# Kernel tuning notes

Measured on AMD Instinct MI355X. Metric: run time of the kernel, lower is better.

## Reference

```python
import jax, jax.numpy as jnp
import numpy as np

NUM_ITERATIONS = 3
LAMBDA_WEIGHT = 0.6
EPS = 1e-8


def _squash(s):
    # s: [N, out_dim]; norm over feature dim (dim=1 in torch, keepdim)
    s_norm = jnp.linalg.norm(s, axis=1, keepdims=True)
    scale = s_norm / (1.0 + s_norm)
    return scale * s / (s_norm + EPS)


def setup_inputs() -> dict:
    key = jax.random.key(0)
    k_h, k_adj, k_w, k_a = jax.random.split(key, 4)
    N, in_dim, out_dim = 4096, 128, 128
    h = jax.random.normal(k_h, (N, in_dim), dtype=jnp.float32)
    adj = jax.random.uniform(k_adj, (N, N), dtype=jnp.float32)
    # xavier_uniform for W [in_dim, out_dim] and attn_a [2*out_dim, 1]
    lim_w = float(np.sqrt(6.0 / (in_dim + out_dim)))
    W = jax.random.uniform(k_w, (in_dim, out_dim), minval=-lim_w, maxval=lim_w, dtype=jnp.float32)
    lim_a = float(np.sqrt(6.0 / (2 * out_dim + 1)))
    attn_a = jax.random.uniform(k_a, (2 * out_dim, 1), minval=-lim_a, maxval=lim_a, dtype=jnp.float32)
    return {"h": h, "adj": adj, "W": W, "attn_a": attn_a}


def reference(h, adj, W, attn_a):
    # Symmetric degree normalization
    d = adj.sum(axis=1) + 1e-8
    d_inv_sqrt = 1.0 / jnp.sqrt(d)
    adj_norm = d_inv_sqrt[:, None] * adj * d_inv_sqrt[None, :]  # [N, N]

    u_hat = h @ W  # [N, out_dim]

    # GAT-style scores via additive decomposition (same math as cat+matmul,
    # avoids the O(N^2 * 2d) h_concat tensor):
    out_dim = W.shape[1]
    a_src = attn_a[:out_dim, 0]  # [in_dim] (in_dim == out_dim)
    a_dst = attn_a[out_dim:, 0]
    attn_scores = (h @ a_src)[:, None] + (h @ a_dst)[None, :]  # [N, N]
    attn_weights = jax.nn.leaky_relu(attn_scores, negative_slope=0.2)

    # Dynamic routing
    b = adj_norm
    c = None
    for it in range(NUM_ITERATIONS):
        c = jax.nn.softmax(b, axis=1)  # [N, N]
        s = c @ u_hat                  # [N, out_dim]
        v = _squash(s)
        if it < NUM_ITERATIONS - 1:
            b = b + v @ u_hat.T        # agreement [N, N]

    combined = LAMBDA_WEIGHT * c + (1.0 - LAMBDA_WEIGHT) * jax.nn.softmax(attn_weights, axis=1)
    s = combined @ u_hat
    return _squash(s)
```

## Files before the change

### kernel.cpp

```cpp
#include <hip/hip_runtime.h>
#include <hip/hip_bf16.h>
#include <math.h>

#define N 4096
#define D 128
#define EPSV 1e-8f

typedef __attribute__((ext_vector_type(8))) short bf16x8;
typedef __attribute__((ext_vector_type(4))) float f32x4;

__device__ __forceinline__ float lrelu(float x){ return x > 0.f ? x : 0.2f*x; }

__device__ __forceinline__ ushort bf16_hi(float x){
  __hip_bfloat16 h = __float2bfloat16(x);
  return *reinterpret_cast<ushort*>(&h);
}
__device__ __forceinline__ float bf16_tof(ushort u){
  __hip_bfloat16 h = *reinterpret_cast<__hip_bfloat16*>(&u);
  return __bfloat162float(h);
}

__device__ __forceinline__ float wave_sum(float v){
  #pragma unroll
  for (int off = 32; off; off >>= 1) v += __shfl_down(v, off);
  return v;
}
__device__ __forceinline__ float block_sum256(float v, float* red){
  v = wave_sum(v);
  if ((threadIdx.x & 63) == 0) red[threadIdx.x >> 6] = v;
  __syncthreads();
  float r = (red[0] + red[1]) + (red[2] + red[3]);
  __syncthreads();
  return r;
}

__global__ void k_rowsum(const float* __restrict__ adj, float* __restrict__ dis){
  int i = blockIdx.x;
  const float4* row = reinterpret_cast<const float4*>(adj + (size_t)i * N);
  float s = 0.f;
  #pragma unroll
  for (int l = 0; l < 4; ++l){
    float4 v = row[threadIdx.x + l * 256];
    s += (v.x + v.y) + (v.z + v.w);
  }
  __shared__ float red[4];
  s = block_sum256(s, red);
  if (threadIdx.x == 0) dis[i] = 1.0f / sqrtf(s + EPSV);
}

__global__ void k_uhat2(const float* __restrict__ h, const float* __restrict__ W,
                        const float* __restrict__ aa,
                        ushort* __restrict__ u_hi, ushort* __restrict__ u_lo,
                        float* __restrict__ p, float* __restrict__ q){
  int i = blockIdx.x, t = threadIdx.x;
  __shared__ float hs[D];
  __shared__ float red[4];
  float hv = h[(size_t)i * D + t];
  hs[t] = hv;
  __syncthreads();
  float acc = 0.f;
  #pragma unroll 8
  for (int k = 0; k < D; ++k) acc = fmaf(hs[k], W[k * D + t], acc);
  ushort hh = bf16_hi(acc);
  u_hi[(size_t)i * D + t] = hh;
  u_lo[(size_t)i * D + t] = bf16_hi(acc - bf16_tof(hh));
  float pv = hv * aa[t];
  float qv = hv * aa[D + t];
  pv = wave_sum(pv); qv = wave_sum(qv);
  if ((t & 63) == 0){ red[t >> 6] = pv; red[2 + (t >> 6)] = qv; }
  __syncthreads();
  if (t == 0){ p[i] = red[0] + red[1]; q[i] = red[2] + red[3]; }
}

__global__ void k_transposeU2(const ushort* __restrict__ u_hi, const ushort* __restrict__ u_lo,
                              ushort* __restrict__ uT_pk){
  __shared__ ushort T[64][136];
  const int tid = threadIdx.x;
  const int j0 = blockIdx.x * 64;
  for (int pass = 0; pass < 2; ++pass){
    const ushort* s = pass ? u_lo : u_hi;
    __syncthreads();
    #pragma unroll
    for (int l = 0; l < 4; ++l){
      int r = l * 16 + (tid >> 4);
      int c = (tid & 15) * 8;
      *reinterpret_cast<uint4*>(&T[r][c]) =
          *reinterpret_cast<const uint4*>(s + (size_t)(j0 + r) * D + c);
    }
    __syncthreads();
    const int dd = tid >> 1, half = tid & 1;
    #pragma unroll
    for (int g = 0; g < 4; ++g){
      int jb = half * 32 + g * 8;
      uint w0 = (uint)T[jb+0][dd] | ((uint)T[jb+1][dd] << 16);
      uint w1 = (uint)T[jb+2][dd] | ((uint)T[jb+3][dd] << 16);
      uint w2 = (uint)T[jb+4][dd] | ((uint)T[jb+5][dd] << 16);
      uint w3 = (uint)T[jb+6][dd] | ((uint)T[jb+7][dd] << 16);
      uint4 w; w.x = w0; w.y = w1; w.z = w2; w.w = w3;
      size_t off = ((size_t)dd * (N/8) + ((j0 + jb) >> 3)) * 16 + pass * 8;
      *reinterpret_cast<uint4*>(uT_pk + off) = w;
    }
  }
}

template<int MODE>
__global__ __launch_bounds__(256, 4)
void k_gemm4(const float* __restrict__ src, const float* __restrict__ dis,
             const float* __restrict__ p, const float* __restrict__ q,
             const ushort* __restrict__ uT_pk,
             float* __restrict__ s_part, float* __restrict__ l_part, int kRange)
{
  const int lane = threadIdx.x & 63;
  const int wave = threadIdx.x >> 6;
  const int row0 = blockIdx.x * 64 + wave * 16;
  const int cl   = lane & 15;
  const int kgrp = (lane >> 4) * 8;
  const int arow = row0 + cl;
  const int k0b  = blockIdx.y * kRange;

  const float dif = (MODE == 0) ? dis[arow] : 0.f;
  const float pi  = (MODE == 2) ? p[arow] : 0.f;
  const float* srow = (MODE == 2) ? q : src + (size_t)arow * N;

  f32x4 acc[8] = {};
  float lsum = 0.f;

  float av[8], dv[8];
  {
    int kk = k0b + kgrp;
    *reinterpret_cast<float4*>(av)     = *reinterpret_cast<const float4*>(srow + kk);
    *reinterpret_cast<float4*>(av + 4) = *reinterpret_cast<const float4*>(srow + kk + 4);
    if (MODE == 0){
      *reinterpret_cast<float4*>(dv)     = *reinterpret_cast<const float4*>(dis + kk);
      *reinterpret_cast<float4*>(dv + 4) = *reinterpret_cast<const float4*>(dis + kk + 4);
    }
  }

  for (int kt = 0; kt < kRange; kt += 32){
    const int kk = k0b + kt + kgrp;
    float4 n0, n1, m0, m1;
    const bool more = (kt + 32 < kRange);
    if (more){
      n0 = *reinterpret_cast<const float4*>(srow + kk + 32);
      n1 = *reinterpret_cast<const float4*>(srow + kk + 36);
      if (MODE == 0){
        m0 = *reinterpret_cast<const float4*>(dis + kk + 32);
        m1 = *reinterpret_cast<const float4*>(dis + kk + 36);
      }
    }
    float ex[8];
    #pragma unroll
    for (int e = 0; e < 8; ++e){
      float x;
      if (MODE == 0)      x = av[e] * dif * dv[e];
      else if (MODE == 1) x = av[e];
      else                x = lrelu(pi + av[e]);
      ex[e] = __expf(x);
      lsum += ex[e];
    }
    bf16x8 ahi, alo;
    #pragma unroll
    for (int e = 0; e < 8; ++e){
      ushort hh = bf16_hi(ex[e]);
      ahi[e] = (short)hh;
      alo[e] = (short)bf16_hi(ex[e] - bf16_tof(hh));
    }
    const size_t kb16 = (size_t)(kk >> 3) * 16;
    #pragma unroll
    for (int ct = 0; ct < 8; ++ct){
      const ushort* bp = uT_pk + (size_t)(ct * 16 + cl) * (N/8) * 16 + kb16;
      bf16x8 bh = *reinterpret_cast<const bf16x8*>(bp);
      bf16x8 bl = *reinterpret_cast<const bf16x8*>(bp + 8);
      acc[ct] = __builtin_amdgcn_mfma_f32_16x16x32_bf16(ahi, bh, acc[ct], 0, 0, 0);
      acc[ct] = __builtin_amdgcn_mfma_f32_16x16x32_bf16(ahi, bl, acc[ct], 0, 0, 0);
      acc[ct] = __builtin_amdgcn_mfma_f32_16x16x32_bf16(alo, bh, acc[ct], 0, 0, 0);
    }
    if (more){
      *reinterpret_cast<float4*>(av)     = n0;
      *reinterpret_cast<float4*>(av + 4) = n1;
      if (MODE == 0){
        *reinterpret_cast<float4*>(dv)     = m0;
        *reinterpret_cast<float4*>(dv + 4) = m1;
      }
    }
  }

  lsum += __shfl_xor(lsum, 16);
  lsum += __shfl_xor(lsum, 32);
  if (lane < 16) l_part[(size_t)blockIdx.y * N + row0 + lane] = lsum;

  const int orow = row0 + (lane >> 4) * 4;
  float* sp = s_part + ((size_t)blockIdx.y * N + orow) * D + cl;
  #pragma unroll
  for (int ct = 0; ct < 8; ++ct)
    #pragma unroll
    for (int r = 0; r < 4; ++r)
      sp[(size_t)r * D + ct * 16] = acc[ct][r];
}

__global__ void k_reduce_attn(const float* __restrict__ s_part, const float* __restrict__ l_part,
                              float* __restrict__ s_attn, float* __restrict__ l_a, int ks){
  int row = blockIdx.x, t = threadIdx.x;
  float a = 0.f;
  for (int y = 0; y < ks; ++y) a += s_part[((size_t)y * N + row) * D + t];
  s_attn[(size_t)row * D + t] = a;
  if (t == 0){
    float la = 0.f;
    for (int y = 0; y < ks; ++y) la += l_part[(size_t)y * N + row];
    l_a[row] = la;
  }
}

template<bool FINAL>
__global__ void k_reduce_squash3(const float* __restrict__ s_part, const float* __restrict__ l_part,
                                 const float* __restrict__ s_attn, const float* __restrict__ l_a,
                                 float* __restrict__ out,
                                 ushort* __restrict__ vh, ushort* __restrict__ vl, int ks){
  int row = blockIdx.x, t = threadIdx.x;
  float a = 0.f;
  for (int y = 0; y < ks; ++y) a += s_part[((size_t)y * N + row) * D + t];
  __shared__ float lbs;
  __shared__ float red[2];
  if (t == 0){
    float lb = 0.f;
    for (int y = 0; y < ks; ++y) lb += l_part[(size_t)y * N + row];
    lbs = lb;
  }
  __syncthreads();
  float val;
  if (FINAL)
    val = 0.6f * a / lbs + 0.4f * s_attn[(size_t)row * D + t] / l_a[row];
  else
    val = a / lbs;
  float ss = wave_sum(val * val);
  if ((t & 63) == 0) red[t >> 6] = ss;
  __syncthreads();
  float tot = red[0] + red[1];
  float n = sqrtf(tot);
  float f = n / ((1.0f + n) * (n + EPSV));
  float o = val * f;
  if (FINAL) out[(size_t)row * D + t] = o;
  else {
    ushort hh = bf16_hi(o);
    vh[(size_t)row * D + t] = hh;
    vl[(size_t)row * D + t] = bf16_hi(o - bf16_tof(hh));
  }
}

template<bool FIRST>
__global__ __launch_bounds__(256, 4)
void k_bupd3(const ushort* __restrict__ v_hi, const ushort* __restrict__ v_lo,
             const ushort* __restrict__ u_hi, const ushort* __restrict__ u_lo,
             const float* __restrict__ adj, const float* __restrict__ dis,
             float* __restrict__ b)
{
  const int lane = threadIdx.x & 63;
  const int wave = threadIdx.x >> 6;
  const int row0 = (blockIdx.x >> 5) * 128 + wave * 32;
  const int col0 = (blockIdx.x & 31) * 128;
  const int cl   = lane & 15;
  const int kgrp = (lane >> 4) * 8;

  f32x4 acc[2][8] = {};

  #pragma unroll
  for (int ks = 0; ks < 4; ++ks){
    const int kk = ks * 32 + kgrp;
    bf16x8 a_h[2], a_l[2];
    #pragma unroll
    for (int rt = 0; rt < 2; ++rt){
      size_t off = (size_t)(row0 + rt * 16 + cl) * D + kk;
      a_h[rt] = *reinterpret_cast<const bf16x8*>(v_hi + off);
      a_l[rt] = *reinterpret_cast<const bf16x8*>(v_lo + off);
    }
    #pragma unroll
    for (int ct = 0; ct < 8; ++ct){
      size_t off = (size_t)(col0 + ct * 16 + cl) * D + kk;
      bf16x8 b_h = *reinterpret_cast<const bf16x8*>(u_hi + off);
      bf16x8 b_l = *reinterpret_cast<const bf16x8*>(u_lo + off);
      #pragma unroll
      for (int rt = 0; rt < 2; ++rt){
        acc[rt][ct] = __builtin_amdgcn_mfma_f32_16x16x32_bf16(a_h[rt], b_h, acc[rt][ct], 0, 0, 0);
        acc[rt][ct] = __builtin_amdgcn_mfma_f32_16x16x32_bf16(a_h[rt], b_l, acc[rt][ct], 0, 0, 0);
        acc[rt][ct] = __builtin_amdgcn_mfma_f32_16x16x32_bf16(a_l[rt], b_h, acc[rt][ct], 0, 0, 0);
      }
    }
  }

  float dcol[8];
  if (FIRST){
    #pragma unroll
    for (int ct = 0; ct < 8; ++ct) dcol[ct] = dis[col0 + ct * 16 + cl];
  }
  #pragma unroll
  for (int rt = 0; rt < 2; ++rt){
    const int orow = row0 + rt * 16 + (lane >> 4) * 4;
    #pragma unroll
    for (int r = 0; r < 4; ++r){
      const int gr = orow + r;
      const float drow = FIRST ? dis[gr] : 0.f;
      size_t base = (size_t)gr * N + col0 + cl;
      #pragma unroll
      for (int ct = 0; ct < 8; ++ct){
        size_t idx = base + ct * 16;
        if (FIRST) b[idx] = fmaf(adj[idx], drow * dcol[ct], acc[rt][ct][r]);
        else       b[idx] += acc[rt][ct][r];
      }
    }
  }
}

extern "C" void kernel_launch(void* const* d_in, const int* in_sizes, int n_in,
                              void* d_out, int out_size, void* d_ws, size_t ws_size,
                              hipStream_t stream) {
  const float* h   = (const float*)d_in[0];
  const float* adj = (const float*)d_in[1];
  const float* W   = (const float*)d_in[2];
  const float* aa  = (const float*)d_in[3];
  float* out = (float*)d_out;
  float* ws  = (float*)d_ws;

  float* dis    = ws;
  float* p      = ws + 4096;
  float* q      = ws + 8192;
  float* l_a    = ws + 12288;
  float* l_part = ws + 16384;
  ushort* u_hi  = (ushort*)(ws + 81920);
  ushort* u_lo  = u_hi  + (size_t)N * D;
  ushort* uT_pk = u_lo  + (size_t)N * D;
  ushort* v_hi  = uT_pk + (size_t)(N/8) * D * 16;
  ushort* v_lo  = v_hi  + (size_t)N * D;
  float* s_attn = (float*)(v_lo + (size_t)N * D);
  float* b      = s_attn + (size_t)N * D;
  float* s_part = b + (size_t)N * N;

  size_t base_floats = (size_t)(s_part - ws);
  int KS = 16;
  while (KS > 1 && (base_floats + (size_t)KS * N * D) * 4 > ws_size) KS >>= 1;
  int kRange = N / KS;
  dim3 gg(64, KS);

  k_rowsum<<<N, 256, 0, stream>>>(adj, dis);
  k_uhat2<<<N, 128, 0, stream>>>(h, W, aa, u_hi, u_lo, p, q);
  k_transposeU2<<<64, 256, 0, stream>>>(u_hi, u_lo, uT_pk);

  k_gemm4<2><<<gg, 256, 0, stream>>>(nullptr, dis, p, q, uT_pk, s_part, l_part, kRange);
  k_reduce_attn<<<N, 128, 0, stream>>>(s_part, l_part, s_attn, l_a, KS);

  k_gemm4<0><<<gg, 256, 0, stream>>>(adj, dis, p, q, uT_pk, s_part, l_part, kRange);
  k_reduce_squash3<false><<<N, 128, 0, stream>>>(s_part, l_part, s_attn, l_a, out, v_hi, v_lo, KS);
  k_bupd3<true><<<1024, 256, 0, stream>>>(v_hi, v_lo, u_hi, u_lo, adj, dis, b);

  k_gemm4<1><<<gg, 256, 0, stream>>>(b, dis, p, q, uT_pk, s_part, l_part, kRange);
  k_reduce_squash3<false><<<N, 128, 0, stream>>>(s_part, l_part, s_attn, l_a, out, v_hi, v_lo, KS);
  k_bupd3<false><<<1024, 256, 0, stream>>>(v_hi, v_lo, u_hi, u_lo, adj, dis, b);

  k_gemm4<1><<<gg, 256, 0, stream>>>(b, dis, p, q, uT_pk, s_part, l_part, kRange);
  k_reduce_squash3<true><<<N, 128, 0, stream>>>(s_part, l_part, s_attn, l_a, out, v_hi, v_lo, KS);
}
```

Baseline: 552.2 us.

## Stage GEMM operands through LDS and coalesce b-update stores via shared transpose

The softmax-GEMM kernel now processes 128 rows per block, cooperatively loading the A tile and the packed U^T tile into shared memory with coalesced loads. Each wave computes two row tiles, so every B fragment is reused twice, and the grid shrinks by half. The b-update kernel stages the V and U hi/lo tiles in LDS and writes results through a padded shared transpose, so global reads and writes of adj and b become coalesced float4 accesses. The cost is extra __syncthreads barriers, more LDS usage, and the loss of the previous register prefetch and explicit occupancy hint.

```diff
diff --git a/kernel.cpp b/kernel.cpp
--- a/kernel.cpp
+++ b/kernel.cpp
@@ -104,98 +104,141 @@
 }
 
 template<int MODE>
-__global__ __launch_bounds__(256, 4)
-void k_gemm4(const float* __restrict__ src, const float* __restrict__ dis,
+__global__ __launch_bounds__(256)
+void k_gemm5(const float* __restrict__ src, const float* __restrict__ dis,
              const float* __restrict__ p, const float* __restrict__ q,
              const ushort* __restrict__ uT_pk,
              float* __restrict__ s_part, float* __restrict__ l_part, int kRange)
 {
-  const int lane = threadIdx.x & 63;
-  const int wave = threadIdx.x >> 6;
-  const int row0 = blockIdx.x * 64 + wave * 16;
+  __shared__ float  As[128][36];
+  __shared__ ushort Bs[128][72];
+
+  const int tid  = threadIdx.x;
+  const int lane = tid & 63;
+  const int wave = tid >> 6;
+  const int row0 = blockIdx.x * 128;
   const int cl   = lane & 15;
   const int kgrp = (lane >> 4) * 8;
-  const int arow = row0 + cl;
   const int k0b  = blockIdx.y * kRange;
 
-  const float dif = (MODE == 0) ? dis[arow] : 0.f;
-  const float pi  = (MODE == 2) ? p[arow] : 0.f;
-  const float* srow = (MODE == 2) ? q : src + (size_t)arow * N;
-
-  f32x4 acc[8] = {};
-  float lsum = 0.f;
-
-  float av[8], dv[8];
-  {
-    int kk = k0b + kgrp;
-    *reinterpret_cast<float4*>(av)     = *reinterpret_cast<const float4*>(srow + kk);
-    *reinterpret_cast<float4*>(av + 4) = *reinterpret_cast<const float4*>(srow + kk + 4);
+  float dif[2], pr[2];
+  #pragma unroll
+  for (int rt = 0; rt < 2; ++rt){
+    int ar = row0 + wave * 32 + rt * 16 + cl;
+    dif[rt] = (MODE == 0) ? dis[ar] : 0.f;
+    pr[rt]  = (MODE == 2) ? p[ar] : 0.f;
+  }
+
+  f32x4 acc[2][8] = {};
+  float lsum[2] = {0.f, 0.f};
+
+  for (int kt = 0; kt < kRange; kt += 32){
+    const int kb = k0b + kt;
+    float4 a_st[4];
+    if (MODE != 2){
+      #pragma unroll
+      for (int i = 0; i < 4; ++i){
+        int idx = i * 256 + tid;
+        int r = idx >> 3, c = idx & 7;
+        a_st[i] = *reinterpret_cast<const float4*>(src + (size_t)(row0 + r) * N + kb + c * 4);
+      }
+    }
+    uint4 b_st[4];
+    const int kb8 = kb >> 3;
+    #pragma unroll
+    for (int i = 0; i < 4; ++i){
+      int idx = i * 256 + tid;
+      int n = idx >> 3, u = idx & 7;
+      b_st[i] = *reinterpret_cast<const uint4*>(
+          uT_pk + (size_t)n * (N/8) * 16 + (size_t)(kb8 + (u & 3)) * 16 + (u >> 2) * 8);
+    }
+    __syncthreads();
+    if (MODE != 2){
+      #pragma unroll
+      for (int i = 0; i < 4; ++i){
+        int idx = i * 256 + tid;
+        int r = idx >> 3, c = idx & 7;
+        *reinterpret_cast<float4*>(&As[r][c * 4]) = a_st[i];
+      }
+    }
+    #pragma unroll
+    for (int i = 0; i < 4; ++i){
+      int idx = i * 256 + tid;
+      int n = idx >> 3, u = idx & 7;
+      *reinterpret_cast<uint4*>(&Bs[n][(u >> 2) * 32 + (u & 3) * 8]) = b_st[i];
+    }
+    __syncthreads();
+
+    float aux[8];
     if (MODE == 0){
-      *reinterpret_cast<float4*>(dv)     = *reinterpret_cast<const float4*>(dis + kk);
-      *reinterpret_cast<float4*>(dv + 4) = *reinterpret_cast<const float4*>(dis + kk + 4);
-    }
-  }
-
-  for (int kt = 0; kt < kRange; kt += 32){
-    const int kk = k0b + kt + kgrp;
-    float4 n0, n1, m0, m1;
-    const bool more = (kt + 32 < kRange);
-    if (more){
-      n0 = *reinterpret_cast<const float4*>(srow + kk + 32);
-      n1 = *reinterpret_cast<const float4*>(srow + kk + 36);
-      if (MODE == 0){
-        m0 = *reinterpret_cast<const float4*>(dis + kk + 32);
-        m1 = *reinterpret_cast<const float4*>(dis + kk + 36);
-      }
-    }
-    float ex[8];
-    #pragma unroll
-    for (int e = 0; e < 8; ++e){
-      float x;
-      if (MODE == 0)      x = av[e] * dif * dv[e];
-      else if (MODE == 1) x = av[e];
-      else                x = lrelu(pi + av[e]);
-      ex[e] = __expf(x);
-      lsum += ex[e];
-    }
-    bf16x8 ahi, alo;
-    #pragma unroll
-    for (int e = 0; e < 8; ++e){
-      ushort hh = bf16_hi(ex[e]);
-      ahi[e] = (short)hh;
-      alo[e] = (short)bf16_hi(ex[e] - bf16_tof(hh));
-    }
-    const size_t kb16 = (size_t)(kk >> 3) * 16;
+      *reinterpret_cast<float4*>(aux)     = *reinterpret_cast<const float4*>(dis + kb + kgrp);
+      *reinterpret_cast<float4*>(aux + 4) = *reinterpret_cast<const float4*>(dis + kb + kgrp + 4);
+    } else if (MODE == 2){
+      *reinterpret_cast<float4*>(aux)     = *reinterpret_cast<const float4*>(q + kb + kgrp);
+      *reinterpret_cast<float4*>(aux + 4) = *reinterpret_cast<const float4*>(q + kb + kgrp + 4);
+    }
+
+    bf16x8 ahi[2], alo[2];
+    #pragma unroll
+    for (int rt = 0; rt < 2; ++rt){
+      float ex[8];
+      if (MODE == 2){
+        #pragma unroll
+        for (int e = 0; e < 8; ++e) ex[e] = __expf(lrelu(pr[rt] + aux[e]));
+      } else {
+        const int rl = wave * 32 + rt * 16 + cl;
+        float av[8];
+        *reinterpret_cast<float4*>(av)     = *reinterpret_cast<const float4*>(&As[rl][kgrp]);
+        *reinterpret_cast<float4*>(av + 4) = *reinterpret_cast<const float4*>(&As[rl][kgrp + 4]);
+        if (MODE == 0){
+          #pragma unroll
+          for (int e = 0; e < 8; ++e) ex[e] = __expf(av[e] * dif[rt] * aux[e]);
+        } else {
+          #pragma unroll
+          for (int e = 0; e < 8; ++e) ex[e] = __expf(av[e]);
+        }
+      }
+      #pragma unroll
+      for (int e = 0; e < 8; ++e){
+        lsum[rt] += ex[e];
+        ushort hh = bf16_hi(ex[e]);
+        ahi[rt][e] = (short)hh;
+        alo[rt][e] = (short)bf16_hi(ex[e] - bf16_tof(hh));
+      }
+    }
+
     #pragma unroll
     for (int ct = 0; ct < 8; ++ct){
-      const ushort* bp = uT_pk + (size_t)(ct * 16 + cl) * (N/8) * 16 + kb16;
-      bf16x8 bh = *reinterpret_cast<const bf16x8*>(bp);
-      bf16x8 bl = *reinterpret_cast<const bf16x8*>(bp + 8);
-      acc[ct] = __builtin_amdgcn_mfma_f32_16x16x32_bf16(ahi, bh, acc[ct], 0, 0, 0);
-      acc[ct] = __builtin_amdgcn_mfma_f32_16x16x32_bf16(ahi, bl, acc[ct], 0, 0, 0);
-      acc[ct] = __builtin_amdgcn_mfma_f32_16x16x32_bf16(alo, bh, acc[ct], 0, 0, 0);
-    }
-    if (more){
-      *reinterpret_cast<float4*>(av)     = n0;
-      *reinterpret_cast<float4*>(av + 4) = n1;
-      if (MODE == 0){
-        *reinterpret_cast<float4*>(dv)     = m0;
-        *reinterpret_cast<float4*>(dv + 4) = m1;
-      }
-    }
-  }
-
-  lsum += __shfl_xor(lsum, 16);
-  lsum += __shfl_xor(lsum, 32);
-  if (lane < 16) l_part[(size_t)blockIdx.y * N + row0 + lane] = lsum;
-
-  const int orow = row0 + (lane >> 4) * 4;
-  float* sp = s_part + ((size_t)blockIdx.y * N + orow) * D + cl;
-  #pragma unroll
-  for (int ct = 0; ct < 8; ++ct)
-    #pragma unroll
-    for (int r = 0; r < 4; ++r)
-      sp[(size_t)r * D + ct * 16] = acc[ct][r];
+      const int col = ct * 16 + cl;
+      bf16x8 bh = *reinterpret_cast<const bf16x8*>(&Bs[col][kgrp]);
+      bf16x8 bl = *reinterpret_cast<const bf16x8*>(&Bs[col][32 + kgrp]);
+      #pragma unroll
+      for (int rt = 0; rt < 2; ++rt){
+        acc[rt][ct] = __builtin_amdgcn_mfma_f32_16x16x32_bf16(ahi[rt], bh, acc[rt][ct], 0, 0, 0);
+        acc[rt][ct] = __builtin_amdgcn_mfma_f32_16x16x32_bf16(ahi[rt], bl, acc[rt][ct], 0, 0, 0);
+        acc[rt][ct] = __builtin_amdgcn_mfma_f32_16x16x32_bf16(alo[rt], bh, acc[rt][ct], 0, 0, 0);
+      }
+    }
+  }
+
+  #pragma unroll
+  for (int rt = 0; rt < 2; ++rt){
+    float l = lsum[rt];
+    l += __shfl_xor(l, 16);
+    l += __shfl_xor(l, 32);
+    if (lane < 16)
+      l_part[(size_t)blockIdx.y * N + row0 + wave * 32 + rt * 16 + lane] = l;
+  }
+  #pragma unroll
+  for (int rt = 0; rt < 2; ++rt){
+    const int orow = row0 + wave * 32 + rt * 16 + (lane >> 4) * 4;
+    float* sp = s_part + ((size_t)blockIdx.y * N + orow) * D + cl;
+    #pragma unroll
+    for (int ct = 0; ct < 8; ++ct)
+      #pragma unroll
+      for (int r = 0; r < 4; ++r)
+        sp[(size_t)r * D + ct * 16] = acc[rt][ct][r];
+  }
 }
 
 __global__ void k_reduce_attn(const float* __restrict__ s_part, const float* __restrict__ l_part,
@@ -248,15 +291,21 @@
 }
 
 template<bool FIRST>
-__global__ __launch_bounds__(256, 4)
-void k_bupd3(const ushort* __restrict__ v_hi, const ushort* __restrict__ v_lo,
+__global__ __launch_bounds__(256)
+void k_bupd5(const ushort* __restrict__ v_hi, const ushort* __restrict__ v_lo,
              const ushort* __restrict__ u_hi, const ushort* __restrict__ u_lo,
              const float* __restrict__ adj, const float* __restrict__ dis,
              float* __restrict__ b)
 {
-  const int lane = threadIdx.x & 63;
-  const int wave = threadIdx.x >> 6;
-  const int row0 = (blockIdx.x >> 5) * 128 + wave * 32;
+  __shared__ __align__(16) char smem[36864];
+  ushort (*vs)[72] = reinterpret_cast<ushort(*)[72]>(smem);
+  ushort (*us)[72] = reinterpret_cast<ushort(*)[72]>(smem + 18432);
+  float*  tr       = reinterpret_cast<float*>(smem);
+
+  const int tid  = threadIdx.x;
+  const int lane = tid & 63;
+  const int wave = tid >> 6;
+  const int row0 = (blockIdx.x >> 5) * 128;
   const int col0 = (blockIdx.x & 31) * 128;
   const int cl   = lane & 15;
   const int kgrp = (lane >> 4) * 8;
@@ -265,19 +314,39 @@
 
   #pragma unroll
   for (int ks = 0; ks < 4; ++ks){
-    const int kk = ks * 32 + kgrp;
+    const int kk = ks * 32;
+    uint4 v_st[4], u_st[4];
+    #pragma unroll
+    for (int i = 0; i < 4; ++i){
+      int idx = i * 256 + tid;
+      int r = idx >> 3, uu = idx & 7;
+      const ushort* vsrc = (uu < 4) ? v_hi : v_lo;
+      v_st[i] = *reinterpret_cast<const uint4*>(vsrc + (size_t)(row0 + r) * D + kk + (uu & 3) * 8);
+      const ushort* usrc = (uu < 4) ? u_hi : u_lo;
+      u_st[i] = *reinterpret_cast<const uint4*>(usrc + (size_t)(col0 + r) * D + kk + (uu & 3) * 8);
+    }
+    __syncthreads();
+    #pragma unroll
+    for (int i = 0; i < 4; ++i){
+      int idx = i * 256 + tid;
+      int r = idx >> 3, uu = idx & 7;
+      *reinterpret_cast<uint4*>(&vs[r][(uu >> 2) * 32 + (uu & 3) * 8]) = v_st[i];
+      *reinterpret_cast<uint4*>(&us[r][(uu >> 2) * 32 + (uu & 3) * 8]) = u_st[i];
+    }
+    __syncthreads();
+
     bf16x8 a_h[2], a_l[2];
     #pragma unroll
     for (int rt = 0; rt < 2; ++rt){
-      size_t off = (size_t)(row0 + rt * 16 + cl) * D + kk;
-      a_h[rt] = *reinterpret_cast<const bf16x8*>(v_hi + off);
-      a_l[rt] = *reinterpret_cast<const bf16x8*>(v_lo + off);
+      const int rl = wave * 32 + rt * 16 + cl;
+      a_h[rt] = *reinterpret_cast<const bf16x8*>(&vs[rl][kgrp]);
+      a_l[rt] = *reinterpret_cast<const bf16x8*>(&vs[rl][32 + kgrp]);
     }
     #pragma unroll
     for (int ct = 0; ct < 8; ++ct){
-      size_t off = (size_t)(col0 + ct * 16 + cl) * D + kk;
-      bf16x8 b_h = *reinterpret_cast<const bf16x8*>(u_hi + off);
-      bf16x8 b_l = *reinterpret_cast<const bf16x8*>(u_lo + off);
+      const int col = ct * 16 + cl;
+      bf16x8 b_h = *reinterpret_cast<const bf16x8*>(&us[col][kgrp]);
+      bf16x8 b_l = *reinterpret_cast<const bf16x8*>(&us[col][32 + kgrp]);
       #pragma unroll
       for (int rt = 0; rt < 2; ++rt){
         acc[rt][ct] = __builtin_amdgcn_mfma_f32_16x16x32_bf16(a_h[rt], b_h, acc[rt][ct], 0, 0, 0);
@@ -285,28 +354,40 @@
         acc[rt][ct] = __builtin_amdgcn_mfma_f32_16x16x32_bf16(a_l[rt], b_h, acc[rt][ct], 0, 0, 0);
       }
     }
-  }
-
-  float dcol[8];
-  if (FIRST){
-    #pragma unroll
-    for (int ct = 0; ct < 8; ++ct) dcol[ct] = dis[col0 + ct * 16 + cl];
-  }
+    __syncthreads();
+  }
+
   #pragma unroll
   for (int rt = 0; rt < 2; ++rt){
-    const int orow = row0 + rt * 16 + (lane >> 4) * 4;
-    #pragma unroll
-    for (int r = 0; r < 4; ++r){
-      const int gr = orow + r;
-      const float drow = FIRST ? dis[gr] : 0.f;
-      size_t base = (size_t)gr * N + col0 + cl;
-      #pragma unroll
-      for (int ct = 0; ct < 8; ++ct){
-        size_t idx = base + ct * 16;
-        if (FIRST) b[idx] = fmaf(adj[idx], drow * dcol[ct], acc[rt][ct][r]);
-        else       b[idx] += acc[rt][ct][r];
-      }
-    }
+    #pragma unroll
+    for (int ct = 0; ct < 8; ++ct)
+      #pragma unroll
+      for (int r = 0; r < 4; ++r)
+        tr[(wave * 16 + (lane >> 4) * 4 + r) * 132 + ct * 16 + cl] = acc[rt][ct][r];
+    __syncthreads();
+    #pragma unroll
+    for (int i = 0; i < 8; ++i){
+      int idx = i * 256 + tid;
+      int rl = idx >> 5, c4 = (idx & 31) * 4;
+      int grow = row0 + (rl >> 4) * 32 + rt * 16 + (rl & 15);
+      float4 v = *reinterpret_cast<const float4*>(&tr[rl * 132 + c4]);
+      size_t gidx = (size_t)grow * N + col0 + c4;
+      float4 o;
+      if (FIRST){
+        float4 ad = *reinterpret_cast<const float4*>(adj + gidx);
+        float dr = dis[grow];
+        float4 dc = *reinterpret_cast<const float4*>(dis + col0 + c4);
+        o.x = fmaf(ad.x, dr * dc.x, v.x);
+        o.y = fmaf(ad.y, dr * dc.y, v.y);
+        o.z = fmaf(ad.z, dr * dc.z, v.z);
+        o.w = fmaf(ad.w, dr * dc.w, v.w);
+      } else {
+        float4 bo = *reinterpret_cast<const float4*>(b + gidx);
+        o.x = bo.x + v.x; o.y = bo.y + v.y; o.z = bo.z + v.z; o.w = bo.w + v.w;
+      }
+      *reinterpret_cast<float4*>(b + gidx) = o;
+    }
+    __syncthreads();
   }
 }
 
@@ -338,23 +419,23 @@
   int KS = 16;
   while (KS > 1 && (base_floats + (size_t)KS * N * D) * 4 > ws_size) KS >>= 1;
   int kRange = N / KS;
-  dim3 gg(64, KS);
+  dim3 gg(32, KS);
 
   k_rowsum<<<N, 256, 0, stream>>>(adj, dis);
   k_uhat2<<<N, 128, 0, stream>>>(h, W, aa, u_hi, u_lo, p, q);
   k_transposeU2<<<64, 256, 0, stream>>>(u_hi, u_lo, uT_pk);
 
-  k_gemm4<2><<<gg, 256, 0, stream>>>(nullptr, dis, p, q, uT_pk, s_part, l_part, kRange);
+  k_gemm5<2><<<gg, 256, 0, stream>>>(nullptr, dis, p, q, uT_pk, s_part, l_part, kRange);
   k_reduce_attn<<<N, 128, 0, stream>>>(s_part, l_part, s_attn, l_a, KS);
 
-  k_gemm4<0><<<gg, 256, 0, stream>>>(adj, dis, p, q, uT_pk, s_part, l_part, kRange);
+  k_gemm5<0><<<gg, 256, 0, stream>>>(adj, dis, p, q, uT_pk, s_part, l_part, kRange);
   k_reduce_squash3<false><<<N, 128, 0, stream>>>(s_part, l_part, s_attn, l_a, out, v_hi, v_lo, KS);
-  k_bupd3<true><<<1024, 256, 0, stream>>>(v_hi, v_lo, u_hi, u_lo, adj, dis, b);
-
-  k_gemm4<1><<<gg, 256, 0, stream>>>(b, dis, p, q, uT_pk, s_part, l_part, kRange);
+  k_bupd5<true><<<1024, 256, 0, stream>>>(v_hi, v_lo, u_hi, u_lo, adj, dis, b);
+
+  k_gemm5<1><<<gg, 256, 0, stream>>>(b, dis, p, q, uT_pk, s_part, l_part, kRange);
   k_reduce_squash3<false><<<N, 128, 0, stream>>>(s_part, l_part, s_attn, l_a, out, v_hi, v_lo, KS);
-  k_bupd3<false><<<1024, 256, 0, stream>>>(v_hi, v_lo, u_hi, u_lo, adj, dis, b);
-
-  k_gemm4<1><<<gg, 256, 0, stream>>>(b, dis, p, q, uT_pk, s_part, l_part, kRange);
+  k_bupd5<false><<<1024, 256, 0, stream>>>(v_hi, v_lo, u_hi, u_lo, adj, dis, b);
+
+  k_gemm5<1><<<gg, 256, 0, stream>>>(b, dis, p, q, uT_pk, s_part, l_part, kRange);
   k_reduce_squash3<true><<<N, 128, 0, stream>>>(s_part, l_part, s_attn, l_a, out, v_hi, v_lo, KS);
 }
```

New measurement: 483.0 us. -12.5%, faster.

## Fuse agreement matrix into softmax GEMM via accumulated v sum, drop b buffer

Applied to the files above, without the earlier changes.

Instead of materializing the N×N logit matrix b and updating it with separate v·uᵀ GEMMs, the routing logits are recomputed on the fly as adj_norm plus (sum of previous v)·uᵀ inside the softmax-GEMM kernel. The reduce kernel keeps a running vsum, which is split into bf16 hi/lo parts. The GEMM now stages adj and packed uᵀ tiles through shared memory. This removes the 64MB b writes and reads and the bupd kernels. In exchange it adds per-tile MFMA recomputation, extra barriers, and a fresh read of adj on every iteration.

```diff
diff --git a/kernel.cpp b/kernel.cpp
--- a/kernel.cpp
+++ b/kernel.cpp
@@ -104,98 +104,160 @@
 }
 
 template<int MODE>
-__global__ __launch_bounds__(256, 4)
-void k_gemm4(const float* __restrict__ src, const float* __restrict__ dis,
+__global__ __launch_bounds__(256)
+void k_gemm6(const float* __restrict__ adj, const float* __restrict__ dis,
              const float* __restrict__ p, const float* __restrict__ q,
              const ushort* __restrict__ uT_pk,
+             const ushort* __restrict__ u_hi, const ushort* __restrict__ u_lo,
+             const ushort* __restrict__ vs_hi, const ushort* __restrict__ vs_lo,
              float* __restrict__ s_part, float* __restrict__ l_part, int kRange)
 {
-  const int lane = threadIdx.x & 63;
-  const int wave = threadIdx.x >> 6;
-  const int row0 = blockIdx.x * 64 + wave * 16;
+  __shared__ float  As[64][36];
+  __shared__ ushort Bs[128][72];
+  __shared__ float  Cs[4][16][36];
+
+  const int tid  = threadIdx.x;
+  const int lane = tid & 63;
+  const int wave = tid >> 6;
+  const int row0 = blockIdx.x * 64;
   const int cl   = lane & 15;
   const int kgrp = (lane >> 4) * 8;
-  const int arow = row0 + cl;
   const int k0b  = blockIdx.y * kRange;
-
-  const float dif = (MODE == 0) ? dis[arow] : 0.f;
-  const float pi  = (MODE == 2) ? p[arow] : 0.f;
-  const float* srow = (MODE == 2) ? q : src + (size_t)arow * N;
+  const int arow_w = row0 + wave * 16;
+
+  const float dif = (MODE < 2) ? dis[arow_w + cl] : 0.f;
+  const float pr  = (MODE == 2) ? p[arow_w + cl] : 0.f;
 
   f32x4 acc[8] = {};
   float lsum = 0.f;
 
-  float av[8], dv[8];
-  {
-    int kk = k0b + kgrp;
-    *reinterpret_cast<float4*>(av)     = *reinterpret_cast<const float4*>(srow + kk);
-    *reinterpret_cast<float4*>(av + 4) = *reinterpret_cast<const float4*>(srow + kk + 4);
-    if (MODE == 0){
-      *reinterpret_cast<float4*>(dv)     = *reinterpret_cast<const float4*>(dis + kk);
-      *reinterpret_cast<float4*>(dv + 4) = *reinterpret_cast<const float4*>(dis + kk + 4);
-    }
-  }
-
   for (int kt = 0; kt < kRange; kt += 32){
-    const int kk = k0b + kt + kgrp;
-    float4 n0, n1, m0, m1;
-    const bool more = (kt + 32 < kRange);
-    if (more){
-      n0 = *reinterpret_cast<const float4*>(srow + kk + 32);
-      n1 = *reinterpret_cast<const float4*>(srow + kk + 36);
-      if (MODE == 0){
-        m0 = *reinterpret_cast<const float4*>(dis + kk + 32);
-        m1 = *reinterpret_cast<const float4*>(dis + kk + 36);
+    const int kb = k0b + kt;
+    float4 a_st[2];
+    if (MODE != 2){
+      #pragma unroll
+      for (int i = 0; i < 2; ++i){
+        int idx = i * 256 + tid;
+        int r = idx >> 3, c = idx & 7;
+        a_st[i] = *reinterpret_cast<const float4*>(adj + (size_t)(row0 + r) * N + kb + c * 4);
       }
     }
+    uint4 b_st[4];
+    const int kb8 = kb >> 3;
+    #pragma unroll
+    for (int i = 0; i < 4; ++i){
+      int idx = i * 256 + tid;
+      int n = idx >> 3, u = idx & 7;
+      b_st[i] = *reinterpret_cast<const uint4*>(
+          uT_pk + (size_t)n * (N/8) * 16 + (size_t)(kb8 + (u & 3)) * 16 + (u >> 2) * 8);
+    }
+    __syncthreads();
+    if (MODE != 2){
+      #pragma unroll
+      for (int i = 0; i < 2; ++i){
+        int idx = i * 256 + tid;
+        int r = idx >> 3, c = idx & 7;
+        *reinterpret_cast<float4*>(&As[r][c * 4]) = a_st[i];
+      }
+    }
+    #pragma unroll
+    for (int i = 0; i < 4; ++i){
+      int idx = i * 256 + tid;
+      int n = idx >> 3, u = idx & 7;
+      *reinterpret_cast<uint4*>(&Bs[n][(u >> 2) * 32 + (u & 3) * 8]) = b_st[i];
+    }
+    __syncthreads();
+
+    if (MODE == 1){
+      f32x4 cacc[2] = {};
+      #pragma unroll
+      for (int kk2 = 0; kk2 < D; kk2 += 32){
+        const size_t voff = (size_t)(arow_w + cl) * D + kk2 + kgrp;
+        bf16x8 vh = *reinterpret_cast<const bf16x8*>(vs_hi + voff);
+        bf16x8 vl = *reinterpret_cast<const bf16x8*>(vs_lo + voff);
+        #pragma unroll
+        for (int nt = 0; nt < 2; ++nt){
+          const size_t uoff = (size_t)(kb + nt * 16 + cl) * D + kk2 + kgrp;
+          bf16x8 uh = *reinterpret_cast<const bf16x8*>(u_hi + uoff);
+          bf16x8 ul = *reinterpret_cast<const bf16x8*>(u_lo + uoff);
+          cacc[nt] = __builtin_amdgcn_mfma_f32_16x16x32_bf16(vh, uh, cacc[nt], 0, 0, 0);
+          cacc[nt] = __builtin_amdgcn_mfma_f32_16x16x32_bf16(vh, ul, cacc[nt], 0, 0, 0);
+          cacc[nt] = __builtin_amdgcn_mfma_f32_16x16x32_bf16(vl, uh, cacc[nt], 0, 0, 0);
+        }
+      }
+      #pragma unroll
+      for (int nt = 0; nt < 2; ++nt)
+        #pragma unroll
+        for (int r = 0; r < 4; ++r)
+          Cs[wave][(lane >> 4) * 4 + r][nt * 16 + cl] = cacc[nt][r];
+      __syncthreads();
+    }
+
+    float aux[8];
+    if (MODE < 2){
+      *reinterpret_cast<float4*>(aux)     = *reinterpret_cast<const float4*>(dis + kb + kgrp);
+      *reinterpret_cast<float4*>(aux + 4) = *reinterpret_cast<const float4*>(dis + kb + kgrp + 4);
+    } else {
+      *reinterpret_cast<float4*>(aux)     = *reinterpret_cast<const float4*>(q + kb + kgrp);
+      *reinterpret_cast<float4*>(aux + 4) = *reinterpret_cast<const float4*>(q + kb + kgrp + 4);
+    }
+
     float ex[8];
+    if (MODE == 2){
+      #pragma unroll
+      for (int e = 0; e < 8; ++e) ex[e] = __expf(lrelu(pr + aux[e]));
+    } else {
+      float av[8];
+      const int rl = wave * 16 + cl;
+      *reinterpret_cast<float4*>(av)     = *reinterpret_cast<const float4*>(&As[rl][kgrp]);
+      *reinterpret_cast<float4*>(av + 4) = *reinterpret_cast<const float4*>(&As[rl][kgrp + 4]);
+      if (MODE == 1){
+        float cv[8];
+        *reinterpret_cast<float4*>(cv)     = *reinterpret_cast<const float4*>(&Cs[wave][cl][kgrp]);
+        *reinterpret_cast<float4*>(cv + 4) = *reinterpret_cast<const float4*>(&Cs[wave][cl][kgrp + 4]);
+        #pragma unroll
+        for (int e = 0; e < 8; ++e) ex[e] = __expf(av[e] * dif * aux[e] + cv[e]);
+      } else {
+        #pragma unroll
+        for (int e = 0; e < 8; ++e) ex[e] = __expf(av[e] * dif * aux[e]);
+      }
+    }
+    bf16x8 ahi, alo;
     #pragma unroll
     for (int e = 0; e < 8; ++e){
-      float x;
-      if (MODE == 0)      x = av[e] * dif * dv[e];
-      else if (MODE == 1) x = av[e];
-      else                x = lrelu(pi + av[e]);
-      ex[e] = __expf(x);
       lsum += ex[e];
-    }
-    bf16x8 ahi, alo;
-    #pragma unroll
-    for (int e = 0; e < 8; ++e){
       ushort hh = bf16_hi(ex[e]);
       ahi[e] = (short)hh;
       alo[e] = (short)bf16_hi(ex[e] - bf16_tof(hh));
     }
-    const size_t kb16 = (size_t)(kk >> 3) * 16;
+
     #pragma unroll
     for (int ct = 0; ct < 8; ++ct){
-      const ushort* bp = uT_pk + (size_t)(ct * 16 + cl) * (N/8) * 16 + kb16;
-      bf16x8 bh = *reinterpret_cast<const bf16x8*>(bp);
-      bf16x8 bl = *reinterpret_cast<const bf16x8*>(bp + 8);
+      const int col = ct * 16 + cl;
+      bf16x8 bh = *reinterpret_cast<const bf16x8*>(&Bs[col][kgrp]);
+      bf16x8 bl = *reinterpret_cast<const bf16x8*>(&Bs[col][32 + kgrp]);
       acc[ct] = __builtin_amdgcn_mfma_f32_16x16x32_bf16(ahi, bh, acc[ct], 0, 0, 0);
       acc[ct] = __builtin_amdgcn_mfma_f32_16x16x32_bf16(ahi, bl, acc[ct], 0, 0, 0);
       acc[ct] = __builtin_amdgcn_mfma_f32_16x16x32_bf16(alo, bh, acc[ct], 0, 0, 0);
     }
-    if (more){
-      *reinterpret_cast<float4*>(av)     = n0;
-      *reinterpret_cast<float4*>(av + 4) = n1;
-      if (MODE == 0){
-        *reinterpret_cast<float4*>(dv)     = m0;
-        *reinterpret_cast<float4*>(dv + 4) = m1;
-      }
-    }
-  }
-
-  lsum += __shfl_xor(lsum, 16);
-  lsum += __shfl_xor(lsum, 32);
-  if (lane < 16) l_part[(size_t)blockIdx.y * N + row0 + lane] = lsum;
-
-  const int orow = row0 + (lane >> 4) * 4;
-  float* sp = s_part + ((size_t)blockIdx.y * N + orow) * D + cl;
-  #pragma unroll
-  for (int ct = 0; ct < 8; ++ct)
-    #pragma unroll
-    for (int r = 0; r < 4; ++r)
-      sp[(size_t)r * D + ct * 16] = acc[ct][r];
+  }
+
+  {
+    float l = lsum;
+    l += __shfl_xor(l, 16);
+    l += __shfl_xor(l, 32);
+    if (lane < 16)
+      l_part[(size_t)blockIdx.y * N + arow_w + lane] = l;
+  }
+  {
+    const int orow = arow_w + (lane >> 4) * 4;
+    float* sp = s_part + ((size_t)blockIdx.y * N + orow) * D + cl;
+    #pragma unroll
+    for (int ct = 0; ct < 8; ++ct)
+      #pragma unroll
+      for (int r = 0; r < 4; ++r)
+        sp[(size_t)r * D + ct * 16] = acc[ct][r];
+  }
 }
 
 __global__ void k_reduce_attn(const float* __restrict__ s_part, const float* __restrict__ l_part,
@@ -211,11 +273,12 @@
   }
 }
 
-template<bool FINAL>
-__global__ void k_reduce_squash3(const float* __restrict__ s_part, const float* __restrict__ l_part,
-                                 const float* __restrict__ s_attn, const float* __restrict__ l_a,
-                                 float* __restrict__ out,
-                                 ushort* __restrict__ vh, ushort* __restrict__ vl, int ks){
+template<int STEP>
+__global__ void k_reduce4(const float* __restrict__ s_part, const float* __restrict__ l_part,
+                          const float* __restrict__ s_attn, const float* __restrict__ l_a,
+                          float* __restrict__ vsum,
+                          ushort* __restrict__ vh, ushort* __restrict__ vl,
+                          float* __restrict__ out, int ks){
   int row = blockIdx.x, t = threadIdx.x;
   float a = 0.f;
   for (int y = 0; y < ks; ++y) a += s_part[((size_t)y * N + row) * D + t];
@@ -227,11 +290,9 @@
     lbs = lb;
   }
   __syncthreads();
-  float val;
-  if (FINAL)
-    val = 0.6f * a / lbs + 0.4f * s_attn[(size_t)row * D + t] / l_a[row];
-  else
-    val = a / lbs;
+  float val = a / lbs;
+  if (STEP == 2)
+    val = 0.6f * val + 0.4f * s_attn[(size_t)row * D + t] / l_a[row];
   float ss = wave_sum(val * val);
   if ((t & 63) == 0) red[t >> 6] = ss;
   __syncthreads();
@@ -239,74 +300,14 @@
   float n = sqrtf(tot);
   float f = n / ((1.0f + n) * (n + EPSV));
   float o = val * f;
-  if (FINAL) out[(size_t)row * D + t] = o;
-  else {
-    ushort hh = bf16_hi(o);
+  if (STEP == 2){
+    out[(size_t)row * D + t] = o;
+  } else {
+    float nv = (STEP == 0) ? o : vsum[(size_t)row * D + t] + o;
+    vsum[(size_t)row * D + t] = nv;
+    ushort hh = bf16_hi(nv);
     vh[(size_t)row * D + t] = hh;
-    vl[(size_t)row * D + t] = bf16_hi(o - bf16_tof(hh));
-  }
-}
-
-template<bool FIRST>
-__global__ __launch_bounds__(256, 4)
-void k_bupd3(const ushort* __restrict__ v_hi, const ushort* __restrict__ v_lo,
-             const ushort* __restrict__ u_hi, const ushort* __restrict__ u_lo,
-             const float* __restrict__ adj, const float* __restrict__ dis,
-             float* __restrict__ b)
-{
-  const int lane = threadIdx.x & 63;
-  const int wave = threadIdx.x >> 6;
-  const int row0 = (blockIdx.x >> 5) * 128 + wave * 32;
-  const int col0 = (blockIdx.x & 31) * 128;
-  const int cl   = lane & 15;
-  const int kgrp = (lane >> 4) * 8;
-
-  f32x4 acc[2][8] = {};
-
-  #pragma unroll
-  for (int ks = 0; ks < 4; ++ks){
-    const int kk = ks * 32 + kgrp;
-    bf16x8 a_h[2], a_l[2];
-    #pragma unroll
-    for (int rt = 0; rt < 2; ++rt){
-      size_t off = (size_t)(row0 + rt * 16 + cl) * D + kk;
-      a_h[rt] = *reinterpret_cast<const bf16x8*>(v_hi + off);
-      a_l[rt] = *reinterpret_cast<const bf16x8*>(v_lo + off);
-    }
-    #pragma unroll
-    for (int ct = 0; ct < 8; ++ct){
-      size_t off = (size_t)(col0 + ct * 16 + cl) * D + kk;
-      bf16x8 b_h = *reinterpret_cast<const bf16x8*>(u_hi + off);
-      bf16x8 b_l = *reinterpret_cast<const bf16x8*>(u_lo + off);
-      #pragma unroll
-      for (int rt = 0; rt < 2; ++rt){
-        acc[rt][ct] = __builtin_amdgcn_mfma_f32_16x16x32_bf16(a_h[rt], b_h, acc[rt][ct], 0, 0, 0);
-        acc[rt][ct] = __builtin_amdgcn_mfma_f32_16x16x32_bf16(a_h[rt], b_l, acc[rt][ct], 0, 0, 0);
-        acc[rt][ct] = __builtin_amdgcn_mfma_f32_16x16x32_bf16(a_l[rt], b_h, acc[rt][ct], 0, 0, 0);
-      }
-    }
-  }
-
-  float dcol[8];
-  if (FIRST){
-    #pragma unroll
-    for (int ct = 0; ct < 8; ++ct) dcol[ct] = dis[col0 + ct * 16 + cl];
-  }
-  #pragma unroll
-  for (int rt = 0; rt < 2; ++rt){
-    const int orow = row0 + rt * 16 + (lane >> 4) * 4;
-    #pragma unroll
-    for (int r = 0; r < 4; ++r){
-      const int gr = orow + r;
-      const float drow = FIRST ? dis[gr] : 0.f;
-      size_t base = (size_t)gr * N + col0 + cl;
-      #pragma unroll
-      for (int ct = 0; ct < 8; ++ct){
-        size_t idx = base + ct * 16;
-        if (FIRST) b[idx] = fmaf(adj[idx], drow * dcol[ct], acc[rt][ct][r]);
-        else       b[idx] += acc[rt][ct][r];
-      }
-    }
+    vl[(size_t)row * D + t] = bf16_hi(nv - bf16_tof(hh));
   }
 }
 
@@ -324,15 +325,15 @@
   float* p      = ws + 4096;
   float* q      = ws + 8192;
   float* l_a    = ws + 12288;
-  float* l_part = ws + 16384;
-  ushort* u_hi  = (ushort*)(ws + 81920);
+  float* vsum   = ws + 16384;
+  float* l_part = vsum + (size_t)N * D;
+  ushort* u_hi  = (ushort*)(l_part + 65536);
   ushort* u_lo  = u_hi  + (size_t)N * D;
   ushort* uT_pk = u_lo  + (size_t)N * D;
-  ushort* v_hi  = uT_pk + (size_t)(N/8) * D * 16;
-  ushort* v_lo  = v_hi  + (size_t)N * D;
-  float* s_attn = (float*)(v_lo + (size_t)N * D);
-  float* b      = s_attn + (size_t)N * D;
-  float* s_part = b + (size_t)N * N;
+  ushort* vs_hi = uT_pk + (size_t)(N/8) * D * 16;
+  ushort* vs_lo = vs_hi + (size_t)N * D;
+  float* s_attn = (float*)(vs_lo + (size_t)N * D);
+  float* s_part = s_attn + (size_t)N * D;
 
   size_t base_floats = (size_t)(s_part - ws);
   int KS = 16;
@@ -344,17 +345,19 @@
   k_uhat2<<<N, 128, 0, stream>>>(h, W, aa, u_hi, u_lo, p, q);
   k_transposeU2<<<64, 256, 0, stream>>>(u_hi, u_lo, uT_pk);
 
-  k_gemm4<2><<<gg, 256, 0, stream>>>(nullptr, dis, p, q, uT_pk, s_part, l_part, kRange);
+  k_gemm6<2><<<gg, 256, 0, stream>>>(adj, dis, p, q, uT_pk, u_hi, u_lo, vs_hi, vs_lo,
+                                     s_part, l_part, kRange);
   k_reduce_attn<<<N, 128, 0, stream>>>(s_part, l_part, s_attn, l_a, KS);
 
-  k_gemm4<0><<<gg, 256, 0, stream>>>(adj, dis, p, q, uT_pk, s_part, l_part, kRange);
-  k_reduce_squash3<false><<<N, 128, 0, stream>>>(s_part, l_part, s_attn, l_a, out, v_hi, v_lo, KS);
-  k_bupd3<true><<<1024, 256, 0, stream>>>(v_hi, v_lo, u_hi, u_lo, adj, dis, b);
-
-  k_gemm4<1><<<gg, 256, 0, stream>>>(b, dis, p, q, uT_pk, s_part, l_part, kRange);
-  k_reduce_squash3<false><<<N, 128, 0, stream>>>(s_part, l_part, s_attn, l_a, out, v_hi, v_lo, KS);
-  k_bupd3<false><<<1024, 256, 0, stream>>>(v_hi, v_lo, u_hi, u_lo, adj, dis, b);
-
-  k_gemm4<1><<<gg, 256, 0, stream>>>(b, dis, p, q, uT_pk, s_part, l_part, kRange);
-  k_reduce_squash3<true><<<N, 128, 0, stream>>>(s_part, l_part, s_attn, l_a, out, v_hi, v_lo, KS);
-}
+  k_gemm6<0><<<gg, 256, 0, stream>>>(adj, dis, p, q, uT_pk, u_hi, u_lo, vs_hi, vs_lo,
+                                     s_part, l_part, kRange);
+  k_reduce4<0><<<N, 128, 0, stream>>>(s_part, l_part, s_attn, l_a, vsum, vs_hi, vs_lo, out, KS);
+
+  k_gemm6<1><<<gg, 256, 0, stream>>>(adj, dis, p, q, uT_pk, u_hi, u_lo, vs_hi, vs_lo,
+                                     s_part, l_part, kRange);
+  k_reduce4<1><<<N, 128, 0, stream>>>(s_part, l_part, s_attn, l_a, vsum, vs_hi, vs_lo, out, KS);
+
+  k_gemm6<1><<<gg, 256, 0, stream>>>(adj, dis, p, q, uT_pk, u_hi, u_lo, vs_hi, vs_lo,
+                                     s_part, l_part, kRange);
+  k_reduce4<2><<<N, 128, 0, stream>>>(s_part, l_part, s_attn, l_a, vsum, vs_hi, vs_lo, out, KS);
+}
```

New measurement: 626.3 us. 1.13x slower.
